# Optimization experiments

Hardware: AMD Instinct MI355X
Metric: run time of the kernel (lower is better)

## Reference

```python
import jax, jax.numpy as jnp
import numpy as np

T, B, I, H = 512, 64, 512, 1024


def _uniform(key, shape, fan_in):
    s = 1.0 / np.sqrt(fan_in)
    return jax.random.uniform(key, shape, jnp.float32, -s, s)


def setup_inputs() -> dict:
    key = jax.random.key(0)
    ks = jax.random.split(key, 17)
    inp = {"x": jax.random.normal(ks[0], (T, B, I), jnp.float32)}
    gates = ["i", "f", "g", "o"]
    k = 1
    for g in gates:  # input->hidden projections
        inp[f"w_i{g}"] = _uniform(ks[k], (H, I), I); k += 1
        inp[f"b_i{g}"] = _uniform(ks[k], (H,), I); k += 1
    for g in gates:  # hidden->hidden projections
        inp[f"w_h{g}"] = _uniform(ks[k], (H, H), H); k += 1
        inp[f"b_h{g}"] = _uniform(ks[k], (H,), H); k += 1
    return inp


def _lstm(x, w_ii, b_ii, w_if, b_if, w_ig, b_ig, w_io, b_io,
          w_hi, b_hi, w_hf, b_hf, w_hg, b_hg, w_ho, b_ho):
    # Precompute all input projections as large batched GEMMs: [T,B,H] each
    xi = jnp.einsum('tbi,hi->tbh', x, w_ii) + b_ii
    xf = jnp.einsum('tbi,hi->tbh', x, w_if) + b_if
    xg = jnp.einsum('tbi,hi->tbh', x, w_ig) + b_ig
    xo = jnp.einsum('tbi,hi->tbh', x, w_io) + b_io

    def step(carry, xs):
        h, c = carry
        xi_t, xf_t, xg_t, xo_t = xs
        i_t = jax.nn.sigmoid(xi_t + h @ w_hi.T + b_hi)
        f_t = jax.nn.sigmoid(xf_t + h @ w_hf.T + b_hf)
        g_t = jnp.tanh(xg_t + h @ w_hg.T + b_hg)
        o_t = jax.nn.sigmoid(xo_t + h @ w_ho.T + b_ho)
        c_n = f_t * c + i_t * g_t
        h_n = o_t * jnp.tanh(c_n)
        return (h_n, c_n), h_n

    h0 = jnp.zeros((x.shape[1], w_hi.shape[0]), x.dtype)
    (h_t, c_t), outputs = jax.lax.scan(step, (h0, h0), (xi, xf, xg, xo))
    return outputs, (h_t, c_t)


def reference(x, w_ii, b_ii, w_if, b_if, w_ig, b_ig, w_io, b_io,
              w_hi, b_hi, w_hf, b_hf, w_hg, b_hg, w_ho, b_ho):
    return _lstm(x, w_ii, b_ii, w_if, b_if, w_ig, b_ig, w_io, b_io,
                 w_hi, b_hi, w_hf, b_hf, w_hg, b_hg, w_ho, b_ho)
```

## Files before the change

### kernel.cpp

```cpp
#include <hip/hip_runtime.h>
#include <stdint.h>

#define TT 512
#define BB 64
#define II 512
#define HH 1024

typedef __attribute__((ext_vector_type(8))) _Float16 half8;
typedef __attribute__((ext_vector_type(4))) float f32x4;

__device__ __forceinline__ float fsig(float x)  { return 1.0f / (1.0f + __expf(-x)); }
__device__ __forceinline__ float ftanh(float x) { return 1.0f - 2.0f / (1.0f + __expf(2.0f * x)); }

#define ZWORDS (4 * 2 * 16 * HH)

__global__ void lstm_init(uint32_t* ws) {
  const uint32_t i = blockIdx.x * 256u + threadIdx.x;
  if (i < ZWORDS) ws[i] = 0u;
}

__global__ __launch_bounds__(256, 1)
void lstm_persist(const float* __restrict__ x,
                  const float* __restrict__ wii, const float* __restrict__ bii,
                  const float* __restrict__ wif_, const float* __restrict__ bif_,
                  const float* __restrict__ wig, const float* __restrict__ big_,
                  const float* __restrict__ wio, const float* __restrict__ bio,
                  const float* __restrict__ whi, const float* __restrict__ bhi,
                  const float* __restrict__ whf, const float* __restrict__ bhf,
                  const float* __restrict__ whg, const float* __restrict__ bhg,
                  const float* __restrict__ who, const float* __restrict__ bho,
                  float* __restrict__ out, uint8_t* __restrict__ ws)
{
  const int tid  = threadIdx.x;
  const int wid  = tid >> 6;
  const int lane = tid & 63;
  const int quad = lane >> 4;
  const int lrow = lane & 15;

  const int wg   = blockIdx.x;
  const int gb   = wg >> 6;
  const int gc   = wg & 63;
  const int b0   = gb << 4;
  const int col0 = gc << 4;

  const float* wi[4] = {wii, wif_, wig, wio};
  const float* wh[4] = {whi, whf, whg, who};
  const float* bi[4] = {bii, bif_, big_, bio};
  const float* bh[4] = {bhi, bhf, bhg, bho};

  uint32_t* zg = (uint32_t*)ws + gb * (2 * 16 * HH);

  const int kb = wid * 384;
  half8 wfrag[12][4];
#pragma unroll
  for (int kk = 0; kk < 12; ++kk) {
    const int k = kb + kk * 32 + quad * 8;
#pragma unroll
    for (int g = 0; g < 4; ++g) {
      const float* wp = (k < II) ? (wi[g] + (size_t)(col0 + lrow) * II + k)
                                 : (wh[g] + (size_t)(col0 + lrow) * HH + (k - II));
      half8 v;
#pragma unroll
      for (int j = 0; j < 8; ++j) v[j] = (_Float16)wp[j];
      wfrag[kk][g] = v;
    }
  }

  uint32_t hmask = 0u;
#pragma unroll
  for (int kk = 0; kk < 12; ++kk)
    if (kb + kk * 32 >= II) hmask |= 1u << kk;

  const int tb   = tid >> 4;
  const int thc  = tid & 15;
  const int gcol = col0 + thc;
  float bias[4];
#pragma unroll
  for (int g = 0; g < 4; ++g) bias[g] = bi[g][gcol] + bh[g][gcol];

  float c = 0.0f, h = 0.0f;

  __shared__ float red[2][16 * 288];

#pragma unroll 1
  for (int t = 0; t < TT; ++t) {
    const uint32_t* zp   = zg + (t & 1) * (16 * HH);
    uint32_t*       zn   = zg + ((t + 1) & 1) * (16 * HH);
    const float*    xrow = x + ((size_t)t * BB + b0 + lrow) * II;
    const uint32_t* zrow = zp + lrow * HH;

    half8 af[12];
#pragma unroll
    for (int kk = 0; kk < 12; ++kk) {
      const int k = kb + kk * 32 + quad * 8;
      if (kb + kk * 32 < II) {
        f32x4 v0 = *(const f32x4*)(xrow + k);
        f32x4 v1 = *(const f32x4*)(xrow + k + 4);
        half8 v;
#pragma unroll
        for (int j = 0; j < 4; ++j) { v[j] = (_Float16)v0[j]; v[4 + j] = (_Float16)v1[j]; }
        af[kk] = v;
      }
    }

    if (t == 0) {
#pragma unroll
      for (int kk = 0; kk < 12; ++kk)
        if (kb + kk * 32 >= II) {
          half8 v;
#pragma unroll
          for (int j = 0; j < 8; ++j) v[j] = (_Float16)0.0f;
          af[kk] = v;
        }
    } else if (hmask) {
      const uint32_t etag = 1u + ((t - 1) & 3u);
      uint32_t pend = hmask;
      int guard = 0;
      for (;;) {
#pragma unroll
        for (int kk = 0; kk < 12; ++kk) {
          if (kb + kk * 32 < II) continue;
          if (pend & (1u << kk)) {
            const int k = kb + kk * 32 + quad * 8;
            const uint64_t* p = (const uint64_t*)(zrow + (k - II));
            union { uint64_t q[4]; uint32_t u[8]; } cv;
            cv.q[0] = __hip_atomic_load(p + 0, __ATOMIC_RELAXED, __HIP_MEMORY_SCOPE_AGENT);
            cv.q[1] = __hip_atomic_load(p + 1, __ATOMIC_RELAXED, __HIP_MEMORY_SCOPE_AGENT);
            cv.q[2] = __hip_atomic_load(p + 2, __ATOMIC_RELAXED, __HIP_MEMORY_SCOPE_AGENT);
            cv.q[3] = __hip_atomic_load(p + 3, __ATOMIC_RELAXED, __HIP_MEMORY_SCOPE_AGENT);
            uint32_t bad = 0u;
#pragma unroll
            for (int j = 0; j < 8; ++j) bad |= (cv.u[j] ^ etag) & 7u;
            if (bad == 0u) {
              half8 v;
#pragma unroll
              for (int j = 0; j < 8; ++j)
                v[j] = (_Float16)__uint_as_float(cv.u[j]);
              af[kk] = v;
              pend &= ~(1u << kk);
            }
          }
        }
        if (__all(pend == 0u)) break;
        if (++guard > (1 << 18)) break;
        __builtin_amdgcn_s_sleep(1);
      }
    }

    f32x4 acc[4];
#pragma unroll
    for (int g = 0; g < 4; ++g) acc[g] = (f32x4){0.f, 0.f, 0.f, 0.f};
#pragma unroll
    for (int kk = 0; kk < 12; ++kk)
#pragma unroll
      for (int g = 0; g < 4; ++g)
        acc[g] = __builtin_amdgcn_mfma_f32_16x16x32_f16(af[kk], wfrag[kk][g], acc[g], 0, 0, 0);

    float* redb = red[t & 1];
#pragma unroll
    for (int g = 0; g < 4; ++g)
#pragma unroll
      for (int r = 0; r < 4; ++r)
        redb[(wid * 4 + g) * 288 + quad * 72 + r * 16 + lrow] = acc[g][r];
    __syncthreads();

    float pre[4];
#pragma unroll
    for (int g = 0; g < 4; ++g) {
      float s = bias[g];
#pragma unroll
      for (int w = 0; w < 4; ++w)
        s += redb[(w * 4 + g) * 288 + (tb >> 2) * 72 + (tb & 3) * 16 + thc];
      pre[g] = s;
    }

    const float it = fsig(pre[0]);
    const float ft = fsig(pre[1]);
    const float gt = ftanh(pre[2]);
    const float ot = fsig(pre[3]);
    c = ft * c + it * gt;
    h = ot * ftanh(c);

    if (t < TT - 1) {
      const uint32_t stag = 1u + (t & 3u);
      __hip_atomic_store(zn + tb * HH + gcol, (__float_as_uint(h) & ~7u) | stag,
                         __ATOMIC_RELAXED, __HIP_MEMORY_SCOPE_AGENT);
    }
    out[((size_t)t * BB + b0 + tb) * HH + gcol] = h;
  }

  out[(size_t)TT * BB * HH + (size_t)(b0 + tb) * HH + gcol] = h;
  out[(size_t)TT * BB * HH + (size_t)BB * HH + (size_t)(b0 + tb) * HH + gcol] = c;
}

extern "C" void kernel_launch(void* const* d_in, const int* in_sizes, int n_in,
                              void* d_out, int out_size, void* d_ws, size_t ws_size,
                              hipStream_t stream) {
  const float* x    = (const float*)d_in[0];
  const float* wii  = (const float*)d_in[1];
  const float* bii  = (const float*)d_in[2];
  const float* wif_ = (const float*)d_in[3];
  const float* bif_ = (const float*)d_in[4];
  const float* wig  = (const float*)d_in[5];
  const float* big_ = (const float*)d_in[6];
  const float* wio  = (const float*)d_in[7];
  const float* bio  = (const float*)d_in[8];
  const float* whi  = (const float*)d_in[9];
  const float* bhi  = (const float*)d_in[10];
  const float* whf  = (const float*)d_in[11];
  const float* bhf  = (const float*)d_in[12];
  const float* whg  = (const float*)d_in[13];
  const float* bhg  = (const float*)d_in[14];
  const float* who  = (const float*)d_in[15];
  const float* bho  = (const float*)d_in[16];

  lstm_init<<<(ZWORDS + 255) / 256, 256, 0, stream>>>((uint32_t*)d_ws);
  lstm_persist<<<256, 256, 0, stream>>>(x, wii, bii, wif_, bif_, wig, big_, wio, bio,
                                        whi, bhi, whf, bhf, whg, bhg, who, bho,
                                        (float*)d_out, (uint8_t*)d_ws);
}
```

Measured before the change: 4.239 ms.

## Process two batch groups per workgroup with interleaved phases on half the grid

Each persistent workgroup now handles two independent 16-row batch groups, alternating a step for group A and then group B, and the grid shrinks from 256 to 128 workgroups. The weight fragments held in registers are shared by both groups. The aim is for the cross-workgroup wait on one group's hidden state to overlap with the other group's compute, and for fewer workgroups to need synchronising. The trade-off is that each workgroup does twice the serial work per timestep, so per-step latency can grow if the spin waits were not the main cost.

```diff
diff --git a/kernel.cpp b/kernel.cpp
--- a/kernel.cpp
+++ b/kernel.cpp
@@ -38,17 +38,19 @@
   const int lrow = lane & 15;
 
   const int wg   = blockIdx.x;
-  const int gb   = wg >> 6;
+  const int pc   = wg >> 6;
   const int gc   = wg & 63;
-  const int b0   = gb << 4;
   const int col0 = gc << 4;
+  const int gbA  = pc * 2,      gbB  = pc * 2 + 1;
+  const int b0A  = gbA << 4,    b0B  = gbB << 4;
 
   const float* wi[4] = {wii, wif_, wig, wio};
   const float* wh[4] = {whi, whf, whg, who};
   const float* bi[4] = {bii, bif_, big_, bio};
   const float* bh[4] = {bhi, bhf, bhg, bho};
 
-  uint32_t* zg = (uint32_t*)ws + gb * (2 * 16 * HH);
+  uint32_t* zgA = (uint32_t*)ws + gbA * (2 * 16 * HH);
+  uint32_t* zgB = (uint32_t*)ws + gbB * (2 * 16 * HH);
 
   const int kb = wid * 384;
   half8 wfrag[12][4];
@@ -66,11 +68,6 @@
     }
   }
 
-  uint32_t hmask = 0u;
-#pragma unroll
-  for (int kk = 0; kk < 12; ++kk)
-    if (kb + kk * 32 >= II) hmask |= 1u << kk;
-
   const int tb   = tid >> 4;
   const int thc  = tid & 15;
   const int gcol = col0 + thc;
@@ -78,14 +75,13 @@
 #pragma unroll
   for (int g = 0; g < 4; ++g) bias[g] = bi[g][gcol] + bh[g][gcol];
 
-  float c = 0.0f, h = 0.0f;
+  float cA = 0.0f, hA = 0.0f, cB = 0.0f, hB = 0.0f;
 
   __shared__ float red[2][16 * 288];
 
-#pragma unroll 1
-  for (int t = 0; t < TT; ++t) {
-    const uint32_t* zp   = zg + (t & 1) * (16 * HH);
-    uint32_t*       zn   = zg + ((t + 1) & 1) * (16 * HH);
+  auto phase = [&](int t, int b0, uint32_t* zgc, float& cs, float& hs, float* redb) {
+    const uint32_t* zp   = zgc + (t & 1) * (16 * HH);
+    uint32_t*       zn   = zgc + ((t + 1) & 1) * (16 * HH);
     const float*    xrow = x + ((size_t)t * BB + b0 + lrow) * II;
     const uint32_t* zrow = zp + lrow * HH;
 
@@ -112,9 +108,12 @@
           for (int j = 0; j < 8; ++j) v[j] = (_Float16)0.0f;
           af[kk] = v;
         }
-    } else if (hmask) {
+    } else if (wid > 0) {
       const uint32_t etag = 1u + ((t - 1) & 3u);
-      uint32_t pend = hmask;
+      uint32_t pend = 0u;
+#pragma unroll
+      for (int kk = 0; kk < 12; ++kk)
+        if (kb + kk * 32 >= II) pend |= 1u << kk;
       int guard = 0;
       for (;;) {
 #pragma unroll
@@ -156,7 +155,6 @@
       for (int g = 0; g < 4; ++g)
         acc[g] = __builtin_amdgcn_mfma_f32_16x16x32_f16(af[kk], wfrag[kk][g], acc[g], 0, 0, 0);
 
-    float* redb = red[t & 1];
 #pragma unroll
     for (int g = 0; g < 4; ++g)
 #pragma unroll
@@ -178,19 +176,27 @@
     const float ft = fsig(pre[1]);
     const float gt = ftanh(pre[2]);
     const float ot = fsig(pre[3]);
-    c = ft * c + it * gt;
-    h = ot * ftanh(c);
+    cs = ft * cs + it * gt;
+    hs = ot * ftanh(cs);
 
     if (t < TT - 1) {
       const uint32_t stag = 1u + (t & 3u);
-      __hip_atomic_store(zn + tb * HH + gcol, (__float_as_uint(h) & ~7u) | stag,
+      __hip_atomic_store(zn + tb * HH + gcol, (__float_as_uint(hs) & ~7u) | stag,
                          __ATOMIC_RELAXED, __HIP_MEMORY_SCOPE_AGENT);
     }
-    out[((size_t)t * BB + b0 + tb) * HH + gcol] = h;
+    out[((size_t)t * BB + b0 + tb) * HH + gcol] = hs;
+  };
+
+#pragma unroll 1
+  for (int t = 0; t < TT; ++t) {
+    phase(t, b0A, zgA, cA, hA, red[0]);
+    phase(t, b0B, zgB, cB, hB, red[1]);
   }
 
-  out[(size_t)TT * BB * HH + (size_t)(b0 + tb) * HH + gcol] = h;
-  out[(size_t)TT * BB * HH + (size_t)BB * HH + (size_t)(b0 + tb) * HH + gcol] = c;
+  out[(size_t)TT * BB * HH + (size_t)(b0A + tb) * HH + gcol] = hA;
+  out[(size_t)TT * BB * HH + (size_t)BB * HH + (size_t)(b0A + tb) * HH + gcol] = cA;
+  out[(size_t)TT * BB * HH + (size_t)(b0B + tb) * HH + gcol] = hB;
+  out[(size_t)TT * BB * HH + (size_t)BB * HH + (size_t)(b0B + tb) * HH + gcol] = cB;
 }
 
 extern "C" void kernel_launch(void* const* d_in, const int* in_sizes, int n_in,
@@ -215,7 +221,7 @@
   const float* bho  = (const float*)d_in[16];
 
   lstm_init<<<(ZWORDS + 255) / 256, 256, 0, stream>>>((uint32_t*)d_ws);
-  lstm_persist<<<256, 256, 0, stream>>>(x, wii, bii, wif_, bif_, wig, big_, wio, bio,
+  lstm_persist<<<128, 256, 0, stream>>>(x, wii, bii, wif_, bif_, wig, big_, wio, bio,
                                         whi, bhi, whf, bhf, whg, bhg, who, bho,
                                         (float*)d_out, (uint8_t*)d_ws);
 }
```

New measurement: 8.153 ms. +92.3%, slower.
